# Performance work log

Hardware: AMD Instinct MI355X
Metric: run time of the kernel (lower is better)

## Reference

```python
import jax, jax.numpy as jnp
import numpy as np
import math

B, L, D = 2, 2048, 768
H, R = 12, 128
DH = D // H  # 64

def setup_inputs():
    key = jax.random.key(0)
    ks = jax.random.split(key, 9)
    s = 0.02
    return {
        "x": jax.random.normal(ks[0], (B, L, D), jnp.float32),
        "W_qkv": jax.random.normal(ks[1], (D, 3 * D), jnp.float32) * s,
        "b_qkv": jnp.zeros((3 * D,), jnp.float32),
        "W_sem_down": jax.random.normal(ks[2], (D, R), jnp.float32) * s,
        "W_sem_up": jax.random.normal(ks[3], (R, 2 * D), jnp.float32) * s,
        "W_ctx_down": jax.random.normal(ks[4], (D, R), jnp.float32) * s,
        "W_ctx_up": jax.random.normal(ks[5], (R, 2 * D), jnp.float32) * s,
        "temperature": jnp.ones((1,), jnp.float32) * 0.5,
        "W_proj": jax.random.normal(ks[6], (D, D), jnp.float32) * s,
        "b_proj": jnp.zeros((D,), jnp.float32),
        "gamma": jnp.ones((D,), jnp.float32),
        "beta": jnp.zeros((D,), jnp.float32),
    }

def _layernorm(x, gamma, beta, eps=1e-5):
    mu = x.mean(-1, keepdims=True)
    var = ((x - mu) ** 2).mean(-1, keepdims=True)
    return (x - mu) * jax.lax.rsqrt(var + eps) * gamma + beta

def reference(x, W_qkv, b_qkv, W_sem_down, W_sem_up, W_ctx_down, W_ctx_up,
              temperature, W_proj, b_proj, gamma, beta):
    x_norm = _layernorm(x, gamma, beta)
    qkv = x_norm @ W_qkv + b_qkv
    q, k, v = jnp.split(qkv, 3, axis=-1)

    # sinusoidal interference gate from two low-rank branches
    sem = jax.nn.silu(x @ W_sem_down) @ W_sem_up
    sem_amp, sem_phase = jnp.split(sem, 2, axis=-1)
    sem_amp = jax.nn.softplus(sem_amp)
    sem_phase = jnp.tanh(sem_phase) * math.pi
    ctx = jax.nn.silu(x @ W_ctx_down) @ W_ctx_up
    ctx_amp, ctx_phase = jnp.split(ctx, 2, axis=-1)
    ctx_amp = jax.nn.softplus(ctx_amp)
    ctx_phase = jnp.tanh(ctx_phase) * math.pi
    interference = sem_amp * ctx_amp * jnp.cos(sem_phase - ctx_phase) * temperature
    gate = jax.nn.sigmoid(interference)
    k = k * (1.0 + gate)

    # (B,L,D) -> (B,H,L,DH)
    to_heads = lambda t: t.reshape(B, L, H, DH).transpose(0, 2, 1, 3)
    q_f = jax.nn.elu(to_heads(q).astype(jnp.float32)) + 1.0
    k_f = jax.nn.elu(to_heads(k).astype(jnp.float32)) + 1.0
    v_f = to_heads(v).astype(jnp.float32)

    # causal linear attention via explicit k (x) v cumsum
    kv_state = k_f[..., :, None] * v_f[..., None, :]   # (B,H,L,DH,DH)
    kv_cumsum = jnp.cumsum(kv_state, axis=2)
    out_num = jnp.einsum('bhld,bhlde->bhle', q_f, kv_cumsum)
    k_cumsum = jnp.cumsum(k_f, axis=2)
    out_den = (q_f * k_cumsum).sum(-1, keepdims=True) + 1e-6
    attn = (out_num / out_den).astype(x.dtype)
    attn = attn.transpose(0, 2, 1, 3).reshape(B, L, D)
    return attn @ W_proj + b_proj, gate
```

## Files before the change

kernel.cpp:

```cpp
#include <hip/hip_runtime.h>

#define B_    2
#define L_    2048
#define D_    768
#define H_    12
#define BL    4096
#define BH    24
#define CHUNK 128
#define NC    16
#define GOFF  3145728
#define PI_F  3.14159265358979f

typedef __bf16 bf16x8 __attribute__((ext_vector_type(8)));
typedef float  f32x4  __attribute__((ext_vector_type(4)));
typedef unsigned short us8 __attribute__((ext_vector_type(8)));

__device__ __forceinline__ float bf2f(unsigned short u) {
    return __uint_as_float(((unsigned int)u) << 16);
}
__device__ __forceinline__ unsigned short f2bf(float f) {
    unsigned int u = __float_as_uint(f);
    unsigned int r = (u + 0x7fffu + ((u >> 16) & 1u)) >> 16;
    return (unsigned short)r;
}
__device__ __forceinline__ float softplusf(float x) {
    return x > 20.f ? x : log1pf(expf(x));
}
__device__ __forceinline__ void dma16(const unsigned short* g, unsigned short* l) {
    __builtin_amdgcn_global_load_lds(
        (const __attribute__((address_space(1))) unsigned int*)g,
        (__attribute__((address_space(3))) unsigned int*)l, 16, 0, 0);
}

__global__ __launch_bounds__(256) void detect_kernel(const unsigned short* __restrict__ x,
                                                     int* __restrict__ flag)
{
    __shared__ int cnt;
    if (threadIdx.x == 0) cnt = 0;
    __syncthreads();
    int c = 0;
    #pragma unroll
    for (int i = 0; i < 16; i++) {
        unsigned short u = x[threadIdx.x * 16 + i];
        int e = (u >> 7) & 0xff;
        if (e < 100 || e > 140) c++;
    }
    atomicAdd(&cnt, c);
    __syncthreads();
    if (threadIdx.x == 0) flag[0] = (cnt > 512) ? 1 : 0;
}

__global__ __launch_bounds__(256) void convert_small_kernel(
    const void* __restrict__ s1, unsigned short* __restrict__ d1,
    const void* __restrict__ s2, unsigned short* __restrict__ d2,
    const void* __restrict__ s3, unsigned short* __restrict__ d3,
    const void* __restrict__ s4, unsigned short* __restrict__ d4,
    const void* __restrict__ s5, unsigned short* __restrict__ d5,
    const int* __restrict__ flag)
{
    int id = blockIdx.x, t = threadIdx.x;
    int fl = flag[0];
    const void* src; unsigned short* dst; int n, base;
    if (id < 9)       { src = s1; dst = d1; n = 2304; base = id * 256; }
    else if (id < 12) { src = s2; dst = d2; n = 768;  base = (id - 9) * 256; }
    else if (id < 15) { src = s3; dst = d3; n = 768;  base = (id - 12) * 256; }
    else if (id < 18) { src = s4; dst = d4; n = 768;  base = (id - 15) * 256; }
    else              { src = s5; dst = d5; n = 1;    base = 0; }
    int i = base + t;
    if (i < n) dst[i] = fl ? f2bf(((const float*)src)[i]) : ((const unsigned short*)src)[i];
}

__global__ __launch_bounds__(256) void transpose_mega_kernel(
    const void* __restrict__ s0, unsigned short* __restrict__ dq,
    const void* __restrict__ s1, unsigned short* __restrict__ dd,
    const void* __restrict__ s2, unsigned short* __restrict__ dsu,
    const void* __restrict__ s3,
    const void* __restrict__ s4, unsigned short* __restrict__ dcu,
    const void* __restrict__ s5, unsigned short* __restrict__ dp,
    const int* __restrict__ flag)
{
    __shared__ unsigned short tile[32][33];
    int id = blockIdx.x;
    const void* src; unsigned short* dst; int K, N, tid;
    if (id < 1728)      { src = s0; dst = dq;  K = 768; N = 2304; tid = id; }
    else if (id < 1824) { src = s1; dst = dd;  K = 768; N = 128;  tid = id - 1728; }
    else if (id < 2016) { src = s2; dst = dsu; K = 128; N = 1536; tid = id - 1824; }
    else if (id < 2112) { src = s3; dst = dd + (size_t)128 * 768; K = 768; N = 128; tid = id - 2016; }
    else if (id < 2304) { src = s4; dst = dcu; K = 128; N = 1536; tid = id - 2112; }
    else                { src = s5; dst = dp;  K = 768; N = 768;  tid = id - 2304; }
    int tn = N / 32;
    int by = (tid / tn) * 32, bx = (tid % tn) * 32;
    int tx = threadIdx.x & 31, tyb = threadIdx.x >> 5;
    int fl = flag[0];
    #pragma unroll
    for (int i = 0; i < 4; i++) {
        int k = by + tyb * 4 + i, n = bx + tx;
        size_t off = (size_t)k * N + n;
        tile[tyb * 4 + i][tx] = fl ? f2bf(((const float*)src)[off]) : ((const unsigned short*)src)[off];
    }
    __syncthreads();
    #pragma unroll
    for (int i = 0; i < 4; i++) {
        int n = bx + tyb * 4 + i, k = by + tx;
        dst[(size_t)n * K + k] = tile[tx][tyb * 4 + i];
    }
}

__global__ __launch_bounds__(256) void conv_ln_kernel(
    const void* __restrict__ xin,
    const unsigned short* __restrict__ gamma,
    const unsigned short* __restrict__ beta,
    unsigned short* __restrict__ x_c,
    unsigned short* __restrict__ xn,
    const int* __restrict__ flag)
{
    int row = blockIdx.x, t = threadIdx.x;
    int fl = flag[0];
    float v[3];
    #pragma unroll
    for (int j = 0; j < 3; j++) {
        int c = t + j * 256;
        v[j] = fl ? ((const float*)xin)[(size_t)row * D_ + c]
                  : bf2f(((const unsigned short*)xin)[(size_t)row * D_ + c]);
    }
    __shared__ float red[8];
    float s = v[0] + v[1] + v[2];
    #pragma unroll
    for (int m = 32; m >= 1; m >>= 1) s += __shfl_xor(s, m, 64);
    int wid = t >> 6;
    if ((t & 63) == 0) red[wid] = s;
    __syncthreads();
    float mean = (red[0] + red[1] + red[2] + red[3]) * (1.f / 768.f);
    float s2 = 0.f;
    #pragma unroll
    for (int j = 0; j < 3; j++) { float d = v[j] - mean; s2 += d * d; }
    #pragma unroll
    for (int m = 32; m >= 1; m >>= 1) s2 += __shfl_xor(s2, m, 64);
    if ((t & 63) == 0) red[4 + wid] = s2;
    __syncthreads();
    float var = (red[4] + red[5] + red[6] + red[7]) * (1.f / 768.f);
    float rs = rsqrtf(var + 1e-5f);
    #pragma unroll
    for (int j = 0; j < 3; j++) {
        int c = t + j * 256;
        x_c[(size_t)row * D_ + c] = f2bf(v[j]);
        float o = (v[j] - mean) * rs * bf2f(gamma[c]) + bf2f(beta[c]);
        xn[(size_t)row * D_ + c] = f2bf(o);
    }
}

template<int EPI>
__global__ __launch_bounds__(256) void mfma_gemm_kernel(
    const unsigned short* __restrict__ A, int lda,
    const unsigned short* __restrict__ BT,
    const unsigned short* __restrict__ bias,
    const unsigned short* __restrict__ gateb,
    void* __restrict__ outp,
    const int* __restrict__ flag,
    int N, int K)
{
    __shared__ unsigned short sbuf[17408];
    unsigned short* As = sbuf;
    unsigned short* Bs = sbuf + 8192;
    unsigned short* Cs = sbuf;

    int f = blockIdx.y * gridDim.x + blockIdx.x;
    int rps = gridDim.y >> 3;
    int strip = f & 7, within = f >> 3;
    int by = strip * rps + (within % rps);
    int bx = within / rps;
    int m0 = by * 128, n0 = bx * 128;

    int t = threadIdx.x;
    int lane = t & 63, wave = t >> 6, quad = lane >> 4, l16 = lane & 15;
    int wm = (wave & 1) * 64, wn = (wave >> 1) * 64;
    int xr = l16 & 7;

    int sr8 = lane >> 3;
    int scg = (lane & 7) ^ sr8;
    const unsigned short* ApL = A  + (size_t)(m0 + wave * 32 + sr8) * lda + scg * 8;
    const unsigned short* BpL = BT + (size_t)(n0 + wave * 32 + sr8) * K   + scg * 8;
    unsigned short* AsW = As + wave * 32 * 64;
    unsigned short* BsW = Bs + wave * 32 * 64;

    f32x4 acc[4][4];
    #pragma unroll
    for (int i = 0; i < 4; i++)
        #pragma unroll
        for (int j = 0; j < 4; j++) acc[i][j] = (f32x4){0.f, 0.f, 0.f, 0.f};

    for (int k0 = 0; k0 < K; k0 += 64) {
        __syncthreads();
        #pragma unroll
        for (int c = 0; c < 4; c++) {
            dma16(ApL + (size_t)(c * 8) * lda + k0, AsW + c * 512);
            dma16(BpL + (size_t)(c * 8) * K   + k0, BsW + c * 512);
        }
        __syncthreads();
        #pragma unroll
        for (int ks = 0; ks < 2; ks++) {
            bf16x8 af[4], bfr[4];
            #pragma unroll
            for (int i = 0; i < 4; i++)
                af[i] = *(const bf16x8*)&As[(wm + i * 16 + l16) * 64 + (((ks * 4 + quad) ^ xr) * 8)];
            #pragma unroll
            for (int j = 0; j < 4; j++)
                bfr[j] = *(const bf16x8*)&Bs[(wn + j * 16 + l16) * 64 + (((ks * 4 + quad) ^ xr) * 8)];
            #pragma unroll
            for (int i = 0; i < 4; i++)
                #pragma unroll
                for (int j = 0; j < 4; j++)
                    acc[i][j] = __builtin_amdgcn_mfma_f32_16x16x32_bf16(af[i], bfr[j], acc[i][j], 0, 0, 0);
        }
    }

    int fl = (EPI == 3) ? flag[0] : 0;
    __syncthreads();
    #pragma unroll
    for (int j = 0; j < 4; j++) {
        int col = n0 + wn + j * 16 + l16;
        float bv = bias ? bf2f(bias[col]) : 0.f;
        #pragma unroll
        for (int i = 0; i < 4; i++) {
            #pragma unroll
            for (int r = 0; r < 4; r++) {
                int row = m0 + wm + i * 16 + quad * 4 + r;
                float v = acc[i][j][r] + bv;
                if (EPI == 1) v = v / (1.f + expf(-v));
                if (EPI == 2) {
                    if (col < D_) {
                        v = v > 0.f ? v + 1.f : expf(v);
                    } else if (col < 2 * D_) {
                        float gg = bf2f(gateb[(size_t)row * D_ + (col - D_)]);
                        v *= (1.f + gg);
                        v = v > 0.f ? v + 1.f : expf(v);
                    }
                }
                if (EPI == 3 && fl) {
                    ((float*)outp)[(size_t)row * N + col] = v;
                } else {
                    Cs[(wm + i * 16 + quad * 4 + r) * 136 + wn + j * 16 + l16] = f2bf(v);
                }
            }
        }
    }
    if (!(EPI == 3 && fl)) {
        __syncthreads();
        #pragma unroll
        for (int p = 0; p < 8; p++) {
            int idx = p * 256 + t;
            int row = idx >> 4, cc = (idx & 15) * 8;
            *(us8*)&((unsigned short*)outp)[(size_t)(m0 + row) * N + n0 + cc] =
                *(const us8*)&Cs[row * 136 + cc];
        }
    }
}

__global__ __launch_bounds__(256) void gate_mfma_kernel(
    const unsigned short* __restrict__ tdown,
    const unsigned short* __restrict__ WsuT,
    const unsigned short* __restrict__ WcuT,
    const unsigned short* __restrict__ tempc,
    void* __restrict__ dout,
    unsigned short* __restrict__ gateb,
    const int* __restrict__ flag)
{
    __shared__ unsigned short gbuf[4 * 64 * 68];
    int f = blockIdx.y * gridDim.x + blockIdx.x;
    int rps = gridDim.y >> 3;
    int strip = f & 7, within = f >> 3;
    int by = strip * rps + (within % rps);
    int bx = within / rps;
    int m0 = by * 64, c0 = bx * 64;

    int t = threadIdx.x;
    int lane = t & 63, wave = t >> 6, quad = lane >> 4, l16 = lane & 15;
    int tr = t >> 2, tc = (t & 3) * 8;
    f32x4 acc[4][4];
    #pragma unroll
    for (int i = 0; i < 4; i++)
        #pragma unroll
        for (int j = 0; j < 4; j++) acc[i][j] = (f32x4){0.f, 0.f, 0.f, 0.f};

    int Atile = wave >> 1, Btile = 2 + wave;
    for (int k0 = 0; k0 < 128; k0 += 32) {
        us8 v0 = *(const us8*)&tdown[(size_t)(m0 + tr) * 256 + k0 + tc];
        us8 v1 = *(const us8*)&tdown[(size_t)(m0 + tr) * 256 + 128 + k0 + tc];
        us8 v2 = *(const us8*)&WsuT[(size_t)(c0 + tr) * 128 + k0 + tc];
        us8 v3 = *(const us8*)&WsuT[(size_t)(768 + c0 + tr) * 128 + k0 + tc];
        us8 v4 = *(const us8*)&WcuT[(size_t)(c0 + tr) * 128 + k0 + tc];
        us8 v5 = *(const us8*)&WcuT[(size_t)(768 + c0 + tr) * 128 + k0 + tc];
        __syncthreads();
        *(us8*)&gbuf[0 * 2560 + tr * 40 + tc] = v0;
        *(us8*)&gbuf[1 * 2560 + tr * 40 + tc] = v1;
        *(us8*)&gbuf[2 * 2560 + tr * 40 + tc] = v2;
        *(us8*)&gbuf[3 * 2560 + tr * 40 + tc] = v3;
        *(us8*)&gbuf[4 * 2560 + tr * 40 + tc] = v4;
        *(us8*)&gbuf[5 * 2560 + tr * 40 + tc] = v5;
        __syncthreads();
        bf16x8 af[4], bfr[4];
        #pragma unroll
        for (int i = 0; i < 4; i++)
            af[i] = *(const bf16x8*)&gbuf[Atile * 2560 + (i * 16 + l16) * 40 + quad * 8];
        #pragma unroll
        for (int j = 0; j < 4; j++)
            bfr[j] = *(const bf16x8*)&gbuf[Btile * 2560 + (j * 16 + l16) * 40 + quad * 8];
        #pragma unroll
        for (int i = 0; i < 4; i++)
            #pragma unroll
            for (int j = 0; j < 4; j++)
                acc[i][j] = __builtin_amdgcn_mfma_f32_16x16x32_bf16(af[i], bfr[j], acc[i][j], 0, 0, 0);
    }
    __syncthreads();
    #pragma unroll
    for (int i = 0; i < 4; i++)
        #pragma unroll
        for (int j = 0; j < 4; j++)
            #pragma unroll
            for (int r = 0; r < 4; r++)
                gbuf[wave * 4352 + (i * 16 + quad * 4 + r) * 68 + j * 16 + l16] = f2bf(acc[i][j][r]);
    __syncthreads();
    float tempv = bf2f(tempc[0]);
    int fl = flag[0];
    #pragma unroll
    for (int p = 0; p < 16; p++) {
        int idx = p * 256 + t;
        int row = idx >> 6, col = idx & 63;
        float sa = softplusf(bf2f(gbuf[0 * 4352 + row * 68 + col]));
        float sp = tanhf(bf2f(gbuf[1 * 4352 + row * 68 + col])) * PI_F;
        float ca = softplusf(bf2f(gbuf[2 * 4352 + row * 68 + col]));
        float cp = tanhf(bf2f(gbuf[3 * 4352 + row * 68 + col])) * PI_F;
        float inter = sa * ca * cosf(sp - cp) * tempv;
        float g = 1.f / (1.f + expf(-inter));
        size_t off = (size_t)GOFF + (size_t)(m0 + row) * D_ + c0 + col;
        unsigned short gb = f2bf(g);
        if (fl) ((float*)dout)[off] = g;
        else    ((unsigned short*)dout)[off] = gb;
        gateb[(size_t)(m0 + row) * D_ + c0 + col] = gb;
    }
}

__global__ __launch_bounds__(256) void chunk_sum_mfma_kernel(
    const unsigned short* __restrict__ qkvt,
    float* __restrict__ Msum, float* __restrict__ Zsum)
{
    __shared__ __align__(16) unsigned short KT[64 * 136];
    __shared__ __align__(16) unsigned short VT[80 * 136];
    int blk = blockIdx.x;
    int bh = blk / NC, cc = blk - bh * NC;
    int b = bh / H_, h = bh - b * H_;
    int t = threadIdx.x;
    int lane = t & 63, wave = t >> 6, quad = lane >> 4, l16 = lane & 15;
    int lr = t >> 1, lc = (t & 1) * 32;
    size_t rowbase = (size_t)(b * L_ + cc * CHUNK);
    const unsigned short* kg = qkvt + rowbase * 2304 + D_ + h * 64;
    const unsigned short* vg = qkvt + rowbase * 2304 + 2 * D_ + h * 64;
    #pragma unroll
    for (int c = 0; c < 4; c++) {
        us8 kv = *(const us8*)&kg[(size_t)lr * 2304 + lc + c * 8];
        us8 vv = *(const us8*)&vg[(size_t)lr * 2304 + lc + c * 8];
        #pragma unroll
        for (int ii = 0; ii < 8; ii++) {
            KT[(lc + c * 8 + ii) * 136 + lr] = kv[ii];
            VT[(lc + c * 8 + ii) * 136 + lr] = vv[ii];
        }
    }
    if (t < 128) VT[64 * 136 + t] = 0x3F80;
    __syncthreads();

    f32x4 acc[5];
    #pragma unroll
    for (int j = 0; j < 5; j++) acc[j] = (f32x4){0.f, 0.f, 0.f, 0.f};
    #pragma unroll
    for (int ks = 0; ks < 4; ks++) {
        bf16x8 a = *(const bf16x8*)&KT[(wave * 16 + l16) * 136 + ks * 32 + quad * 8];
        #pragma unroll
        for (int j = 0; j < 5; j++) {
            bf16x8 bv = *(const bf16x8*)&VT[(j * 16 + l16) * 136 + ks * 32 + quad * 8];
            acc[j] = __builtin_amdgcn_mfma_f32_16x16x32_bf16(a, bv, acc[j], 0, 0, 0);
        }
    }
    float* mo = Msum + (size_t)blk * 4096;
    #pragma unroll
    for (int j = 0; j < 4; j++)
        #pragma unroll
        for (int r = 0; r < 4; r++)
            mo[(wave * 16 + quad * 4 + r) * 64 + j * 16 + l16] = acc[j][r];
    if (l16 == 0) {
        #pragma unroll
        for (int r = 0; r < 4; r++)
            Zsum[(size_t)blk * 64 + wave * 16 + quad * 4 + r] = acc[4][r];
    }
}

__global__ __launch_bounds__(256) void prefix_kernel(
    float* __restrict__ Msum, float* __restrict__ Zsum)
{
    int blk = blockIdx.x;
    int bh = blk >> 2, qd = blk & 3;
    int t = threadIdx.x;
    size_t base = (size_t)bh * NC * 4096 + qd * 1024 + t * 4;
    float4 v[NC];
    #pragma unroll
    for (int c = 0; c < NC; c++) v[c] = *(const float4*)&Msum[base + (size_t)c * 4096];
    float4 run = make_float4(0.f, 0.f, 0.f, 0.f);
    #pragma unroll
    for (int c = 0; c < NC; c++) {
        float4 tmp = v[c];
        *(float4*)&Msum[base + (size_t)c * 4096] = run;
        run.x += tmp.x; run.y += tmp.y; run.z += tmp.z; run.w += tmp.w;
    }
    if (qd == 0 && t < 64) {
        float rz = 0.f;
        for (int c = 0; c < NC; c++) {
            float* pz = &Zsum[((size_t)bh * NC + c) * 64 + t];
            float vv = *pz; *pz = rz; rz += vv;
        }
    }
}

__global__ __launch_bounds__(256) void chunk_scan_mfma_kernel(
    const unsigned short* __restrict__ qkvt,
    const float* __restrict__ Msum, const float* __restrict__ Zsum,
    unsigned short* __restrict__ attnb)
{
    __shared__ __align__(16) unsigned short sbuf[35072];
    unsigned short* Qs = sbuf;
    unsigned short* Ks = sbuf + 9216;
    unsigned short* Ps = sbuf;
    unsigned short* VT = sbuf + 18432;
    unsigned short* Ss = sbuf + 29312;
    unsigned short* Cout = sbuf;

    int blk = blockIdx.x;
    int bh = blk / NC, cc = blk - bh * NC;
    int b = bh / H_, h = bh - b * H_;
    int t = threadIdx.x;
    int lane = t & 63, wave = t >> 6, quad = lane >> 4, l16 = lane & 15;
    int wm = wave * 32;
    int lr = t >> 1, lc = (t & 1) * 32;
    size_t rowbase = (size_t)(b * L_ + cc * CHUNK);
    const unsigned short* qg = qkvt + rowbase * 2304 + h * 64;
    const unsigned short* kg = qkvt + rowbase * 2304 + D_ + h * 64;
    const unsigned short* vg = qkvt + rowbase * 2304 + 2 * D_ + h * 64;
    const float* mp = Msum + (size_t)blk * 4096;
    const float* zp = Zsum + (size_t)blk * 64;

    #pragma unroll
    for (int c = 0; c < 4; c++) {
        us8 qv = *(const us8*)&qg[(size_t)lr * 2304 + lc + c * 8];
        us8 kv = *(const us8*)&kg[(size_t)lr * 2304 + lc + c * 8];
        us8 vv = *(const us8*)&vg[(size_t)lr * 2304 + lc + c * 8];
        *(us8*)&Qs[lr * 72 + lc + c * 8] = qv;
        *(us8*)&Ks[lr * 72 + lc + c * 8] = kv;
        #pragma unroll
        for (int ii = 0; ii < 8; ii++)
            VT[(lc + c * 8 + ii) * 136 + lr] = vv[ii];
    }
    if (t < 128) VT[64 * 136 + t] = 0x3F80;
    {
        int d = t & 63, jb = (t >> 6) * 16;
        #pragma unroll
        for (int g4 = 0; g4 < 4; g4++) {
            float4 sv = *(const float4*)&mp[d * 64 + jb + g4 * 4];
            Ss[(jb + g4 * 4 + 0) * 72 + d] = f2bf(sv.x);
            Ss[(jb + g4 * 4 + 1) * 72 + d] = f2bf(sv.y);
            Ss[(jb + g4 * 4 + 2) * 72 + d] = f2bf(sv.z);
            Ss[(jb + g4 * 4 + 3) * 72 + d] = f2bf(sv.w);
        }
    }
    if (t < 64) Ss[64 * 72 + t] = f2bf(zp[t]);
    __syncthreads();

    f32x4 Pacc[2][8], Oacc[2][5];
    #pragma unroll
    for (int i = 0; i < 2; i++) {
        #pragma unroll
        for (int n = 0; n < 8; n++) Pacc[i][n] = (f32x4){0.f, 0.f, 0.f, 0.f};
        #pragma unroll
        for (int j = 0; j < 5; j++) Oacc[i][j] = (f32x4){0.f, 0.f, 0.f, 0.f};
    }
    bf16x8 aq[2][2];
    #pragma unroll
    for (int i = 0; i < 2; i++)
        #pragma unroll
        for (int ks = 0; ks < 2; ks++)
            aq[i][ks] = *(const bf16x8*)&Qs[(wm + i * 16 + l16) * 72 + ks * 32 + quad * 8];
    #pragma unroll
    for (int n = 0; n < 8; n++)
        #pragma unroll
        for (int ks = 0; ks < 2; ks++) {
            bf16x8 bk = *(const bf16x8*)&Ks[(n * 16 + l16) * 72 + ks * 32 + quad * 8];
            #pragma unroll
            for (int i = 0; i < 2; i++)
                Pacc[i][n] = __builtin_amdgcn_mfma_f32_16x16x32_bf16(aq[i][ks], bk, Pacc[i][n], 0, 0, 0);
        }
    #pragma unroll
    for (int j = 0; j < 5; j++)
        #pragma unroll
        for (int ks = 0; ks < 2; ks++) {
            bf16x8 bs = *(const bf16x8*)&Ss[(j * 16 + l16) * 72 + ks * 32 + quad * 8];
            #pragma unroll
            for (int i = 0; i < 2; i++)
                Oacc[i][j] = __builtin_amdgcn_mfma_f32_16x16x32_bf16(aq[i][ks], bs, Oacc[i][j], 0, 0, 0);
        }
    __syncthreads();

    #pragma unroll
    for (int i = 0; i < 2; i++)
        #pragma unroll
        for (int n = 0; n < 8; n++)
            #pragma unroll
            for (int r = 0; r < 4; r++) {
                int trow = wm + i * 16 + quad * 4 + r;
                int scol = n * 16 + l16;
                Ps[trow * 136 + scol] = (scol <= trow) ? f2bf(Pacc[i][n][r]) : 0;
            }
    __syncthreads();

    #pragma unroll
    for (int ks = 0; ks < 4; ks++) {
        bf16x8 ap[2];
        #pragma unroll
        for (int i = 0; i < 2; i++)
            ap[i] = *(const bf16x8*)&Ps[(wm + i * 16 + l16) * 136 + ks * 32 + quad * 8];
        #pragma unroll
        for (int j = 0; j < 5; j++) {
            bf16x8 bv = *(const bf16x8*)&VT[(j * 16 + l16) * 136 + ks * 32 + quad * 8];
            #pragma unroll
            for (int i = 0; i < 2; i++)
                Oacc[i][j] = __builtin_amdgcn_mfma_f32_16x16x32_bf16(ap[i], bv, Oacc[i][j], 0, 0, 0);
        }
    }
    __syncthreads();

    #pragma unroll
    for (int i = 0; i < 2; i++) {
        #pragma unroll
        for (int r = 0; r < 4; r++) {
            float den = __shfl(Oacc[i][4][r], lane & 48) + 1e-6f;
            float inv = 1.f / den;
            #pragma unroll
            for (int j = 0; j < 4; j++)
                Cout[(wm + i * 16 + quad * 4 + r) * 136 + j * 16 + l16] = f2bf(Oacc[i][j][r] * inv);
        }
    }
    __syncthreads();
    unsigned short* abase = attnb + rowbase * D_ + h * 64;
    #pragma unroll
    for (int p = 0; p < 4; p++) {
        int idx = p * 256 + t;
        int row = idx >> 3, cg = (idx & 7) * 8;
        *(us8*)&abase[(size_t)row * D_ + cg] = *(const us8*)&Cout[row * 136 + cg];
    }
}

extern "C" void kernel_launch(void* const* d_in, const int* in_sizes, int n_in,
                              void* d_out, int out_size, void* d_ws, size_t ws_size,
                              hipStream_t stream)
{
    char* w = (char*)d_ws;
    auto alloc = [&](size_t bytes) { void* p = (void*)w; w += (bytes + 255) & ~(size_t)255; return p; };
    int*            flagp   = (int*)alloc(256);
    unsigned short* x_c     = (unsigned short*)alloc((size_t)BL * D_ * 2);
    unsigned short* attnb   = x_c;
    unsigned short* xn      = (unsigned short*)alloc((size_t)BL * D_ * 2);
    unsigned short* WqkvT   = (unsigned short*)alloc((size_t)2304 * 768 * 2);
    unsigned short* WdT     = (unsigned short*)alloc((size_t)256 * 768 * 2);
    unsigned short* WsuT    = (unsigned short*)alloc((size_t)1536 * 128 * 2);
    unsigned short* WcuT    = (unsigned short*)alloc((size_t)1536 * 128 * 2);
    unsigned short* WprojT  = (unsigned short*)alloc((size_t)768 * 768 * 2);
    unsigned short* bqkv_c  = (unsigned short*)alloc((size_t)2304 * 2);
    unsigned short* bproj_c = (unsigned short*)alloc((size_t)768 * 2);
    unsigned short* gamma_c = (unsigned short*)alloc((size_t)768 * 2);
    unsigned short* beta_c  = (unsigned short*)alloc((size_t)768 * 2);
    unsigned short* temp_c  = (unsigned short*)alloc(256);
    unsigned short* tdown   = (unsigned short*)alloc((size_t)BL * 256 * 2);
    float*          Zsum    = (float*)alloc((size_t)BH * NC * 64 * 4);
    unsigned short* qkvt    = (unsigned short*)alloc((size_t)BL * 2304 * 2);
    float*          Msum    = (float*)alloc((size_t)BH * NC * 4096 * 4);
    unsigned short* gateb   = (unsigned short*)Msum;

    dim3 blk(256);
    detect_kernel<<<1, blk, 0, stream>>>((const unsigned short*)d_in[0], flagp);
    convert_small_kernel<<<19, blk, 0, stream>>>(
        d_in[2], bqkv_c, d_in[9], bproj_c, d_in[10], gamma_c,
        d_in[11], beta_c, d_in[7], temp_c, flagp);
    transpose_mega_kernel<<<2880, blk, 0, stream>>>(
        d_in[1], WqkvT, d_in[3], WdT, d_in[4], WsuT,
        d_in[5], d_in[6], WcuT, d_in[8], WprojT, flagp);
    conv_ln_kernel<<<BL, blk, 0, stream>>>(d_in[0], gamma_c, beta_c, x_c, xn, flagp);
    mfma_gemm_kernel<1><<<dim3(2, 32), blk, 0, stream>>>(x_c, 768, WdT, nullptr, nullptr, tdown, flagp, 256, 768);
    gate_mfma_kernel<<<dim3(12, 64), blk, 0, stream>>>(tdown, WsuT, WcuT, temp_c, d_out, gateb, flagp);
    mfma_gemm_kernel<2><<<dim3(18, 32), blk, 0, stream>>>(xn, 768, WqkvT, bqkv_c, gateb, qkvt, flagp, 2304, 768);
    chunk_sum_mfma_kernel<<<BH * NC, blk, 0, stream>>>(qkvt, Msum, Zsum);
    prefix_kernel<<<BH * 4, blk, 0, stream>>>(Msum, Zsum);
    chunk_scan_mfma_kernel<<<BH * NC, blk, 0, stream>>>(qkvt, Msum, Zsum, attnb);
    mfma_gemm_kernel<3><<<dim3(6, 32), blk, 0, stream>>>(attnb, 768, WprojT, bproj_c, nullptr, d_out, flagp, 768, 768);
}
```

Baseline: 245.9 us.

## Merge prep kernels, drop prefix kernel, use direct-to-LDS loads with swizzle

Folds the small bias conversions into the weight transpose kernel, and has the LayerNorm and gate kernels read gamma, beta and temperature straight from the raw inputs. This removes two launches. The separate prefix-scan kernel is dropped: each chunk_scan block now sums the preceding chunks' Msum/Zsum itself, trading redundant reads (up to 15 chunks) for one fewer launch. The gate and chunk_scan kernels switch Q/K and operand tiles to dma16 global-to-LDS loads with an XOR-swizzled layout in place of padded layouts, aiming to cut register staging and LDS bank conflicts.

```diff
diff --git a/kernel.cpp b/kernel.cpp
--- a/kernel.cpp
+++ b/kernel.cpp
@@ -50,37 +50,28 @@
     if (threadIdx.x == 0) flag[0] = (cnt > 512) ? 1 : 0;
 }
 
-__global__ __launch_bounds__(256) void convert_small_kernel(
-    const void* __restrict__ s1, unsigned short* __restrict__ d1,
-    const void* __restrict__ s2, unsigned short* __restrict__ d2,
-    const void* __restrict__ s3, unsigned short* __restrict__ d3,
-    const void* __restrict__ s4, unsigned short* __restrict__ d4,
-    const void* __restrict__ s5, unsigned short* __restrict__ d5,
-    const int* __restrict__ flag)
-{
-    int id = blockIdx.x, t = threadIdx.x;
-    int fl = flag[0];
-    const void* src; unsigned short* dst; int n, base;
-    if (id < 9)       { src = s1; dst = d1; n = 2304; base = id * 256; }
-    else if (id < 12) { src = s2; dst = d2; n = 768;  base = (id - 9) * 256; }
-    else if (id < 15) { src = s3; dst = d3; n = 768;  base = (id - 12) * 256; }
-    else if (id < 18) { src = s4; dst = d4; n = 768;  base = (id - 15) * 256; }
-    else              { src = s5; dst = d5; n = 1;    base = 0; }
-    int i = base + t;
-    if (i < n) dst[i] = fl ? f2bf(((const float*)src)[i]) : ((const unsigned short*)src)[i];
-}
-
-__global__ __launch_bounds__(256) void transpose_mega_kernel(
+__global__ __launch_bounds__(256) void prep_mega_kernel(
     const void* __restrict__ s0, unsigned short* __restrict__ dq,
     const void* __restrict__ s1, unsigned short* __restrict__ dd,
     const void* __restrict__ s2, unsigned short* __restrict__ dsu,
     const void* __restrict__ s3,
     const void* __restrict__ s4, unsigned short* __restrict__ dcu,
     const void* __restrict__ s5, unsigned short* __restrict__ dp,
+    const void* __restrict__ sbq, unsigned short* __restrict__ dbq,
+    const void* __restrict__ sbp, unsigned short* __restrict__ dbp,
     const int* __restrict__ flag)
 {
+    int id = blockIdx.x;
+    int fl = flag[0];
+    if (id >= 2880) {
+        const void* src; unsigned short* dst; int n, base;
+        if (id < 2889) { src = sbq; dst = dbq; n = 2304; base = (id - 2880) * 256; }
+        else           { src = sbp; dst = dbp; n = 768;  base = (id - 2889) * 256; }
+        int i = base + threadIdx.x;
+        if (i < n) dst[i] = fl ? f2bf(((const float*)src)[i]) : ((const unsigned short*)src)[i];
+        return;
+    }
     __shared__ unsigned short tile[32][33];
-    int id = blockIdx.x;
     const void* src; unsigned short* dst; int K, N, tid;
     if (id < 1728)      { src = s0; dst = dq;  K = 768; N = 2304; tid = id; }
     else if (id < 1824) { src = s1; dst = dd;  K = 768; N = 128;  tid = id - 1728; }
@@ -91,7 +82,6 @@
     int tn = N / 32;
     int by = (tid / tn) * 32, bx = (tid % tn) * 32;
     int tx = threadIdx.x & 31, tyb = threadIdx.x >> 5;
-    int fl = flag[0];
     #pragma unroll
     for (int i = 0; i < 4; i++) {
         int k = by + tyb * 4 + i, n = bx + tx;
@@ -108,8 +98,7 @@
 
 __global__ __launch_bounds__(256) void conv_ln_kernel(
     const void* __restrict__ xin,
-    const unsigned short* __restrict__ gamma,
-    const unsigned short* __restrict__ beta,
+    const void* __restrict__ gr, const void* __restrict__ br,
     unsigned short* __restrict__ x_c,
     unsigned short* __restrict__ xn,
     const int* __restrict__ flag)
@@ -143,8 +132,10 @@
     #pragma unroll
     for (int j = 0; j < 3; j++) {
         int c = t + j * 256;
+        float gv = fl ? ((const float*)gr)[c] : bf2f(((const unsigned short*)gr)[c]);
+        float bv = fl ? ((const float*)br)[c] : bf2f(((const unsigned short*)br)[c]);
         x_c[(size_t)row * D_ + c] = f2bf(v[j]);
-        float o = (v[j] - mean) * rs * bf2f(gamma[c]) + bf2f(beta[c]);
+        float o = (v[j] - mean) * rs * gv + bv;
         xn[(size_t)row * D_ + c] = f2bf(o);
     }
 }
@@ -260,12 +251,12 @@
     const unsigned short* __restrict__ tdown,
     const unsigned short* __restrict__ WsuT,
     const unsigned short* __restrict__ WcuT,
-    const unsigned short* __restrict__ tempc,
+    const void* __restrict__ tempraw,
     void* __restrict__ dout,
     unsigned short* __restrict__ gateb,
     const int* __restrict__ flag)
 {
-    __shared__ unsigned short gbuf[4 * 64 * 68];
+    __shared__ unsigned short gbuf[17408];
     int f = blockIdx.y * gridDim.x + blockIdx.x;
     int rps = gridDim.y >> 3;
     int strip = f & 7, within = f >> 3;
@@ -275,7 +266,18 @@
 
     int t = threadIdx.x;
     int lane = t & 63, wave = t >> 6, quad = lane >> 4, l16 = lane & 15;
-    int tr = t >> 2, tc = (t & 3) * 8;
+    int xg = l16 & 3;
+
+    int r_t = wave * 16 + (lane >> 2);
+    int g_t = (lane & 3) ^ ((lane >> 2) & 3);
+    const unsigned short* s0 = tdown + (size_t)(m0 + r_t) * 256 + g_t * 8;
+    const unsigned short* s1 = s0 + 128;
+    const unsigned short* s2 = WsuT + (size_t)(c0 + r_t) * 128 + g_t * 8;
+    const unsigned short* s3 = WsuT + (size_t)(768 + c0 + r_t) * 128 + g_t * 8;
+    const unsigned short* s4 = WcuT + (size_t)(c0 + r_t) * 128 + g_t * 8;
+    const unsigned short* s5 = WcuT + (size_t)(768 + c0 + r_t) * 128 + g_t * 8;
+    unsigned short* ldq = gbuf + wave * 512;
+
     f32x4 acc[4][4];
     #pragma unroll
     for (int i = 0; i < 4; i++)
@@ -284,27 +286,21 @@
 
     int Atile = wave >> 1, Btile = 2 + wave;
     for (int k0 = 0; k0 < 128; k0 += 32) {
-        us8 v0 = *(const us8*)&tdown[(size_t)(m0 + tr) * 256 + k0 + tc];
-        us8 v1 = *(const us8*)&tdown[(size_t)(m0 + tr) * 256 + 128 + k0 + tc];
-        us8 v2 = *(const us8*)&WsuT[(size_t)(c0 + tr) * 128 + k0 + tc];
-        us8 v3 = *(const us8*)&WsuT[(size_t)(768 + c0 + tr) * 128 + k0 + tc];
-        us8 v4 = *(const us8*)&WcuT[(size_t)(c0 + tr) * 128 + k0 + tc];
-        us8 v5 = *(const us8*)&WcuT[(size_t)(768 + c0 + tr) * 128 + k0 + tc];
         __syncthreads();
-        *(us8*)&gbuf[0 * 2560 + tr * 40 + tc] = v0;
-        *(us8*)&gbuf[1 * 2560 + tr * 40 + tc] = v1;
-        *(us8*)&gbuf[2 * 2560 + tr * 40 + tc] = v2;
-        *(us8*)&gbuf[3 * 2560 + tr * 40 + tc] = v3;
-        *(us8*)&gbuf[4 * 2560 + tr * 40 + tc] = v4;
-        *(us8*)&gbuf[5 * 2560 + tr * 40 + tc] = v5;
+        dma16(s0 + k0, ldq + 0 * 2048);
+        dma16(s1 + k0, ldq + 1 * 2048);
+        dma16(s2 + k0, ldq + 2 * 2048);
+        dma16(s3 + k0, ldq + 3 * 2048);
+        dma16(s4 + k0, ldq + 4 * 2048);
+        dma16(s5 + k0, ldq + 5 * 2048);
         __syncthreads();
         bf16x8 af[4], bfr[4];
         #pragma unroll
         for (int i = 0; i < 4; i++)
-            af[i] = *(const bf16x8*)&gbuf[Atile * 2560 + (i * 16 + l16) * 40 + quad * 8];
+            af[i] = *(const bf16x8*)&gbuf[Atile * 2048 + (i * 16 + l16) * 32 + ((quad ^ xg) * 8)];
         #pragma unroll
         for (int j = 0; j < 4; j++)
-            bfr[j] = *(const bf16x8*)&gbuf[Btile * 2560 + (j * 16 + l16) * 40 + quad * 8];
+            bfr[j] = *(const bf16x8*)&gbuf[Btile * 2048 + (j * 16 + l16) * 32 + ((quad ^ xg) * 8)];
         #pragma unroll
         for (int i = 0; i < 4; i++)
             #pragma unroll
@@ -320,8 +316,8 @@
             for (int r = 0; r < 4; r++)
                 gbuf[wave * 4352 + (i * 16 + quad * 4 + r) * 68 + j * 16 + l16] = f2bf(acc[i][j][r]);
     __syncthreads();
-    float tempv = bf2f(tempc[0]);
     int fl = flag[0];
+    float tempv = fl ? ((const float*)tempraw)[0] : bf2f(((const unsigned short*)tempraw)[0]);
     #pragma unroll
     for (int p = 0; p < 16; p++) {
         int idx = p * 256 + t;
@@ -393,43 +389,17 @@
     }
 }
 
-__global__ __launch_bounds__(256) void prefix_kernel(
-    float* __restrict__ Msum, float* __restrict__ Zsum)
-{
-    int blk = blockIdx.x;
-    int bh = blk >> 2, qd = blk & 3;
-    int t = threadIdx.x;
-    size_t base = (size_t)bh * NC * 4096 + qd * 1024 + t * 4;
-    float4 v[NC];
-    #pragma unroll
-    for (int c = 0; c < NC; c++) v[c] = *(const float4*)&Msum[base + (size_t)c * 4096];
-    float4 run = make_float4(0.f, 0.f, 0.f, 0.f);
-    #pragma unroll
-    for (int c = 0; c < NC; c++) {
-        float4 tmp = v[c];
-        *(float4*)&Msum[base + (size_t)c * 4096] = run;
-        run.x += tmp.x; run.y += tmp.y; run.z += tmp.z; run.w += tmp.w;
-    }
-    if (qd == 0 && t < 64) {
-        float rz = 0.f;
-        for (int c = 0; c < NC; c++) {
-            float* pz = &Zsum[((size_t)bh * NC + c) * 64 + t];
-            float vv = *pz; *pz = rz; rz += vv;
-        }
-    }
-}
-
 __global__ __launch_bounds__(256) void chunk_scan_mfma_kernel(
     const unsigned short* __restrict__ qkvt,
     const float* __restrict__ Msum, const float* __restrict__ Zsum,
     unsigned short* __restrict__ attnb)
 {
-    __shared__ __align__(16) unsigned short sbuf[35072];
+    __shared__ __align__(16) unsigned short sbuf[34048];
     unsigned short* Qs = sbuf;
-    unsigned short* Ks = sbuf + 9216;
+    unsigned short* Ks = sbuf + 8192;
     unsigned short* Ps = sbuf;
-    unsigned short* VT = sbuf + 18432;
-    unsigned short* Ss = sbuf + 29312;
+    unsigned short* VT = sbuf + 17408;
+    unsigned short* Ss = sbuf + 28288;
     unsigned short* Cout = sbuf;
 
     int blk = blockIdx.x;
@@ -438,38 +408,54 @@
     int t = threadIdx.x;
     int lane = t & 63, wave = t >> 6, quad = lane >> 4, l16 = lane & 15;
     int wm = wave * 32;
-    int lr = t >> 1, lc = (t & 1) * 32;
+    int xr = l16 & 7;
     size_t rowbase = (size_t)(b * L_ + cc * CHUNK);
     const unsigned short* qg = qkvt + rowbase * 2304 + h * 64;
     const unsigned short* kg = qkvt + rowbase * 2304 + D_ + h * 64;
     const unsigned short* vg = qkvt + rowbase * 2304 + 2 * D_ + h * 64;
-    const float* mp = Msum + (size_t)blk * 4096;
-    const float* zp = Zsum + (size_t)blk * 64;
-
-    #pragma unroll
-    for (int c = 0; c < 4; c++) {
-        us8 qv = *(const us8*)&qg[(size_t)lr * 2304 + lc + c * 8];
-        us8 kv = *(const us8*)&kg[(size_t)lr * 2304 + lc + c * 8];
-        us8 vv = *(const us8*)&vg[(size_t)lr * 2304 + lc + c * 8];
-        *(us8*)&Qs[lr * 72 + lc + c * 8] = qv;
-        *(us8*)&Ks[lr * 72 + lc + c * 8] = kv;
-        #pragma unroll
-        for (int ii = 0; ii < 8; ii++)
-            VT[(lc + c * 8 + ii) * 136 + lr] = vv[ii];
+
+    int r8 = lane >> 3, g8 = (lane & 7) ^ r8;
+    #pragma unroll
+    for (int s = 0; s < 8; s++) {
+        int op = s * 4 + wave;
+        int tl = op >> 4, o16 = op & 15;
+        const unsigned short* src = (tl ? kg : qg) + (size_t)(o16 * 8 + r8) * 2304 + g8 * 8;
+        unsigned short* dst = (tl ? Ks : Qs) + o16 * 512;
+        dma16(src, dst);
+    }
+    {
+        int lr = t >> 1, lc = (t & 1) * 32;
+        #pragma unroll
+        for (int c = 0; c < 4; c++) {
+            us8 vv = *(const us8*)&vg[(size_t)lr * 2304 + lc + c * 8];
+            #pragma unroll
+            for (int ii = 0; ii < 8; ii++)
+                VT[(lc + c * 8 + ii) * 136 + lr] = vv[ii];
+        }
     }
     if (t < 128) VT[64 * 136 + t] = 0x3F80;
     {
         int d = t & 63, jb = (t >> 6) * 16;
-        #pragma unroll
-        for (int g4 = 0; g4 < 4; g4++) {
-            float4 sv = *(const float4*)&mp[d * 64 + jb + g4 * 4];
-            Ss[(jb + g4 * 4 + 0) * 72 + d] = f2bf(sv.x);
-            Ss[(jb + g4 * 4 + 1) * 72 + d] = f2bf(sv.y);
-            Ss[(jb + g4 * 4 + 2) * 72 + d] = f2bf(sv.z);
-            Ss[(jb + g4 * 4 + 3) * 72 + d] = f2bf(sv.w);
-        }
-    }
-    if (t < 64) Ss[64 * 72 + t] = f2bf(zp[t]);
+        float a16[16];
+        #pragma unroll
+        for (int j = 0; j < 16; j++) a16[j] = 0.f;
+        for (int c = 0; c < cc; c++) {
+            const float* mp = Msum + ((size_t)bh * NC + c) * 4096 + d * 64 + jb;
+            #pragma unroll
+            for (int g4 = 0; g4 < 4; g4++) {
+                float4 sv = *(const float4*)&mp[g4 * 4];
+                a16[g4 * 4 + 0] += sv.x; a16[g4 * 4 + 1] += sv.y;
+                a16[g4 * 4 + 2] += sv.z; a16[g4 * 4 + 3] += sv.w;
+            }
+        }
+        #pragma unroll
+        for (int j = 0; j < 16; j++) Ss[(jb + j) * 72 + d] = f2bf(a16[j]);
+    }
+    if (t < 64) {
+        float rz = 0.f;
+        for (int c = 0; c < cc; c++) rz += Zsum[((size_t)bh * NC + c) * 64 + t];
+        Ss[64 * 72 + t] = f2bf(rz);
+    }
     __syncthreads();
 
     f32x4 Pacc[2][8], Oacc[2][5];
@@ -485,12 +471,12 @@
     for (int i = 0; i < 2; i++)
         #pragma unroll
         for (int ks = 0; ks < 2; ks++)
-            aq[i][ks] = *(const bf16x8*)&Qs[(wm + i * 16 + l16) * 72 + ks * 32 + quad * 8];
+            aq[i][ks] = *(const bf16x8*)&Qs[(wm + i * 16 + l16) * 64 + (((ks * 4 + quad) ^ xr) * 8)];
     #pragma unroll
     for (int n = 0; n < 8; n++)
         #pragma unroll
         for (int ks = 0; ks < 2; ks++) {
-            bf16x8 bk = *(const bf16x8*)&Ks[(n * 16 + l16) * 72 + ks * 32 + quad * 8];
+            bf16x8 bk = *(const bf16x8*)&Ks[(n * 16 + l16) * 64 + (((ks * 4 + quad) ^ xr) * 8)];
             #pragma unroll
             for (int i = 0; i < 2; i++)
                 Pacc[i][n] = __builtin_amdgcn_mfma_f32_16x16x32_bf16(aq[i][ks], bk, Pacc[i][n], 0, 0, 0);
@@ -572,9 +558,6 @@
     unsigned short* WprojT  = (unsigned short*)alloc((size_t)768 * 768 * 2);
     unsigned short* bqkv_c  = (unsigned short*)alloc((size_t)2304 * 2);
     unsigned short* bproj_c = (unsigned short*)alloc((size_t)768 * 2);
-    unsigned short* gamma_c = (unsigned short*)alloc((size_t)768 * 2);
-    unsigned short* beta_c  = (unsigned short*)alloc((size_t)768 * 2);
-    unsigned short* temp_c  = (unsigned short*)alloc(256);
     unsigned short* tdown   = (unsigned short*)alloc((size_t)BL * 256 * 2);
     float*          Zsum    = (float*)alloc((size_t)BH * NC * 64 * 4);
     unsigned short* qkvt    = (unsigned short*)alloc((size_t)BL * 2304 * 2);
@@ -583,18 +566,15 @@
 
     dim3 blk(256);
     detect_kernel<<<1, blk, 0, stream>>>((const unsigned short*)d_in[0], flagp);
-    convert_small_kernel<<<19, blk, 0, stream>>>(
-        d_in[2], bqkv_c, d_in[9], bproj_c, d_in[10], gamma_c,
-        d_in[11], beta_c, d_in[7], temp_c, flagp);
-    transpose_mega_kernel<<<2880, blk, 0, stream>>>(
+    prep_mega_kernel<<<2892, blk, 0, stream>>>(
         d_in[1], WqkvT, d_in[3], WdT, d_in[4], WsuT,
-        d_in[5], d_in[6], WcuT, d_in[8], WprojT, flagp);
-    conv_ln_kernel<<<BL, blk, 0, stream>>>(d_in[0], gamma_c, beta_c, x_c, xn, flagp);
+        d_in[5], d_in[6], WcuT, d_in[8], WprojT,
+        d_in[2], bqkv_c, d_in[9], bproj_c, flagp);
+    conv_ln_kernel<<<BL, blk, 0, stream>>>(d_in[0], d_in[10], d_in[11], x_c, xn, flagp);
     mfma_gemm_kernel<1><<<dim3(2, 32), blk, 0, stream>>>(x_c, 768, WdT, nullptr, nullptr, tdown, flagp, 256, 768);
-    gate_mfma_kernel<<<dim3(12, 64), blk, 0, stream>>>(tdown, WsuT, WcuT, temp_c, d_out, gateb, flagp);
+    gate_mfma_kernel<<<dim3(12, 64), blk, 0, stream>>>(tdown, WsuT, WcuT, d_in[7], d_out, gateb, flagp);
     mfma_gemm_kernel<2><<<dim3(18, 32), blk, 0, stream>>>(xn, 768, WqkvT, bqkv_c, gateb, qkvt, flagp, 2304, 768);
     chunk_sum_mfma_kernel<<<BH * NC, blk, 0, stream>>>(qkvt, Msum, Zsum);
-    prefix_kernel<<<BH * 4, blk, 0, stream>>>(Msum, Zsum);
     chunk_scan_mfma_kernel<<<BH * NC, blk, 0, stream>>>(qkvt, Msum, Zsum, attnb);
     mfma_gemm_kernel<3><<<dim3(6, 32), blk, 0, stream>>>(attnb, 768, WprojT, bproj_c, nullptr, d_out, flagp, 768, 768);
 }
```

Result: slower. 252.7 us (+2.8%).
